# Optimization experiments

Hardware: AMD Instinct MI355X
Metric: run time of the kernel (lower is better)

## Reference

```python
import jax, jax.numpy as jnp
import numpy as np
import math


def setup_inputs() -> dict:
    key = jax.random.key(0)
    ks = jax.random.split(key, 8)
    B, C, H, W = 8, 512, 48, 48
    Cq = C // 8
    s = 0.05
    return {
        "x": jax.random.normal(ks[0], (B, C, H, W), jnp.float32),
        "Wq": jax.random.normal(ks[1], (Cq, C), jnp.float32) * s,
        "bq": jax.random.normal(ks[2], (Cq,), jnp.float32) * s,
        "Wk": jax.random.normal(ks[3], (Cq, C), jnp.float32) * s,
        "bk": jax.random.normal(ks[4], (Cq,), jnp.float32) * s,
        "Wv": jax.random.normal(ks[5], (C, C), jnp.float32) * s,
        "bv": jax.random.normal(ks[6], (C,), jnp.float32) * s,
        "gamma": jax.random.normal(ks[7], (1,), jnp.float32),
    }


def reference(x, Wq, bq, Wk, bk, Wv, bv, gamma):
    B, C, H, W = x.shape
    Cq = Wq.shape[0]
    N = H * W
    xf = x.reshape(B, C, N)  # 1x1 conv == channel matmul
    q = jnp.einsum('oc,bcn->bno', Wq, xf) + bq  # [B, N, Cq] (proj_query, permuted)
    k = jnp.einsum('oc,bcn->bon', Wk, xf) + bk[None, :, None]  # [B, Cq, N]
    v = jnp.einsum('oc,bcn->bon', Wv, xf) + bv[None, :, None]  # [B, C, N]
    # ave_I = (1/Cq)*(I - (1/Cq)*J); Q @ ave_I = (Q - rowmean(Q)) / Cq
    qc = (q - jnp.mean(q, axis=-1, keepdims=True)) / Cq
    sigma = jnp.einsum('bnc,bcm->bnm', qc, k) / math.sqrt(Cq)  # [B, N, N]
    attention = jax.nn.softmax(sigma, axis=-1)
    # out = V @ attention^T : out[b,c,n] = sum_m v[b,c,m] * attention[b,n,m]
    am = jnp.einsum('bcm,bnm->bcn', v, attention).reshape(B, C, H, W)
    out = gamma[0] * am + x
    return out
```

## Files before the change

kernel.cpp:

```cpp
#include <hip/hip_runtime.h>

#define B_ 8
#define C_ 512
#define N_ 2304
#define CQ 64

typedef float f32x4 __attribute__((ext_vector_type(4)));
typedef float f32x16 __attribute__((ext_vector_type(16)));
typedef short bf16x8 __attribute__((ext_vector_type(8)));
typedef unsigned short u16x4 __attribute__((ext_vector_type(4)));
typedef unsigned short u16x8 __attribute__((ext_vector_type(8)));
typedef int i32x4 __attribute__((ext_vector_type(4)));

__device__ __forceinline__ unsigned short f2bf(float f){
  union { float f; unsigned int u; } v; v.f = f;
  unsigned int r = (v.u + 0x7fffu + ((v.u >> 16) & 1u)) >> 16;
  return (unsigned short)r;
}

__device__ __forceinline__ void gload_lds16(const void* g, void* l){
  __builtin_amdgcn_global_load_lds(
      (const __attribute__((address_space(1))) unsigned int*)g,
      (__attribute__((address_space(3))) unsigned int*)l, 16, 0, 0);
}

__global__ __launch_bounds__(256) void k_wcvt(const float* __restrict__ Wq,
                                              const float* __restrict__ Wk,
                                              const float* __restrict__ Wv,
                                              unsigned short* __restrict__ Wb){
  int idx = blockIdx.x*256 + threadIdx.x;
  int h = idx & 1, ln = (idx >> 1) & 31, cs = (idx >> 6) & 31, ob = idx >> 11;
  int row = ob*32 + ln, col = cs*16 + h*8;
  const float* src;
  if (row < 64)       src = Wq + (size_t)row*512 + col;
  else if (row < 128) src = Wk + (size_t)(row-64)*512 + col;
  else                src = Wv + (size_t)(row-128)*512 + col;
  f32x4 v0 = *(const f32x4*)src;
  f32x4 v1 = *(const f32x4*)(src + 4);
  u16x8 o;
  #pragma unroll
  for (int j = 0; j < 4; j++){ o[j] = f2bf(v0[j]); o[4+j] = f2bf(v1[j]); }
  *(u16x8*)(Wb + (size_t)idx*8) = o;
}

__global__ __launch_bounds__(512) void k_prep(const float* __restrict__ x,
                                              const float* __restrict__ bq,
                                              const float* __restrict__ bk,
                                              const float* __restrict__ bv,
                                              const unsigned short* __restrict__ Wb,
                                              unsigned short* __restrict__ qw,
                                              unsigned short* __restrict__ kw,
                                              unsigned short* __restrict__ vw){
  __shared__ short xt_l[32*520];
  __shared__ float scr[2*32*68];

  int i = blockIdx.x; int b = i & 7; int nt = i >> 3;
  int n0 = nt*32;
  int t = threadIdx.x; int w = t >> 6; int l = t & 63;
  int h = l >> 5, ln = l & 31;
  const size_t bN = (size_t)b*N_;

  #pragma unroll
  for (int it = 0; it < 8; it++){
    int c = it*64 + (t >> 3);
    int n4 = (t & 7)*4;
    f32x4 v = *(const f32x4*)(x + ((size_t)b*C_ + c)*N_ + n0 + n4);
    #pragma unroll
    for (int j = 0; j < 4; j++) xt_l[(n4+j)*520 + c] = (short)f2bf(v[j]);
  }
  __syncthreads();

  const unsigned short* wlane = Wb + (size_t)(ln*2 + h)*8;
  const unsigned short* wv0 = wlane + (size_t)(4 + 2*w)*16384;
  const unsigned short* wv1 = wlane + (size_t)(5 + 2*w)*16384;
  const unsigned short* wqk = wlane + (size_t)w*16384;

  f32x16 vacc[2]; f32x16 qkacc;
  #pragma unroll
  for (int rr = 0; rr < 16; rr++){ vacc[0][rr]=0.f; vacc[1][rr]=0.f; qkacc[rr]=0.f; }

  #pragma unroll 8
  for (int cs = 0; cs < 32; cs++){
    bf16x8 bx = *(const bf16x8*)&xt_l[ln*520 + cs*16 + h*8];
    bf16x8 a0 = *(const bf16x8*)(wv0 + (size_t)cs*512);
    bf16x8 a1 = *(const bf16x8*)(wv1 + (size_t)cs*512);
    vacc[0] = __builtin_amdgcn_mfma_f32_32x32x16_bf16(a0, bx, vacc[0], 0, 0, 0);
    vacc[1] = __builtin_amdgcn_mfma_f32_32x32x16_bf16(a1, bx, vacc[1], 0, 0, 0);
    if (w < 4){
      bf16x8 aq = *(const bf16x8*)(wqk + (size_t)cs*512);
      qkacc = __builtin_amdgcn_mfma_f32_32x32x16_bf16(aq, bx, qkacc, 0, 0, 0);
    }
  }

  if (w < 4){
    float* s = scr + ((w >> 1) ? 2176 : 0);
    int obase = (w & 1)*32;
    #pragma unroll
    for (int rr = 0; rr < 16; rr++){
      int o = obase + (rr & 3) + 8*(rr >> 2) + 4*h;
      s[ln*68 + o] = qkacc[rr];
    }
  }
  __syncthreads();

  if (t < 256){
    int isK = t >> 7;
    int tt = t & 127;
    int n = tt >> 2, j = tt & 3;
    const float* s = scr + (isK ? 2176 : 0);
    const float* bias = isK ? bk : bq;
    float vals[16]; float sm = 0.f;
    #pragma unroll
    for (int ii = 0; ii < 16; ii++){
      vals[ii] = s[n*68 + j*16 + ii] + bias[j*16 + ii];
      sm += vals[ii];
    }
    sm += __shfl_xor(sm, 1); sm += __shfl_xor(sm, 2);
    float mean = isK ? 0.f : sm * (1.f/64.f);
    float scl  = isK ? 1.f : (1.44269504089f/512.f);
    u16x8 h0, h1;
    #pragma unroll
    for (int ii = 0; ii < 8; ii++) h0[ii] = f2bf((vals[ii]   - mean)*scl);
    #pragma unroll
    for (int ii = 0; ii < 8; ii++) h1[ii] = f2bf((vals[8+ii] - mean)*scl);
    unsigned short* d = (isK ? kw : qw) + (bN + n0 + n)*CQ + j*16;
    *(u16x8*)d = h0;
    *(u16x8*)(d + 8) = h1;
  }
  __syncthreads();

  #pragma unroll
  for (int r = 0; r < 4; r++){
    if ((w >> 1) == r){
      float* s = scr + (w & 1)*2176;
      #pragma unroll
      for (int of = 0; of < 2; of++)
        #pragma unroll
        for (int rr = 0; rr < 16; rr++){
          int o = of*32 + (rr & 3) + 8*(rr >> 2) + 4*h;
          s[ln*68 + o] = vacc[of][rr];
        }
    }
    __syncthreads();
    {
      int ch = t >> 8;
      int tt = t & 255;
      int o = tt >> 2, jj = (tt >> 1) & 1, half = tt & 1;
      int og = (2*r + ch)*64 + o;
      const float* s = scr + ch*2176;
      float bvv = bv[og];
      u16x8 hv;
      #pragma unroll
      for (int ii = 0; ii < 8; ii++){
        int q2 = ((ii & 3) | ((ii & 4) << 1)) + half*4;
        hv[ii] = f2bf(s[(jj*16 + q2)*68 + o] + bvv);
      }
      *(u16x8*)(vw + ((size_t)b*C_ + og)*N_ + n0 + jj*16 + half*8) = hv;
    }
    __syncthreads();
  }
}

__global__ __launch_bounds__(256) void k_sexp(const unsigned short* __restrict__ qw,
                                              const unsigned short* __restrict__ kw,
                                              unsigned short* __restrict__ Pl,
                                              float* __restrict__ lsum_part,
                                              int b0, int bsh){
  int bid = blockIdx.x;
  int bl = bid & ((1 << bsh) - 1);
  int b = b0 + bl;
  int r = bid >> bsh;
  int ms = r & 3; int nt = r >> 2;
  int t = threadIdx.x; int w = t >> 6; int l = t & 63;
  int h = l >> 5, ln = l & 31;
  int nf = w & 1, mh = w >> 1;
  int n = nt*64 + nf*32 + ln;

  const unsigned short* qb = qw + ((size_t)b*N_ + n)*CQ + h*8;
  bf16x8 qf[4];
  #pragma unroll
  for (int kq = 0; kq < 4; kq++) qf[kq] = *(const bf16x8*)(qb + kq*16);

  int mb32base = ms*18 + mh*9;
  const unsigned short* ks0 = kw + ((size_t)b*N_ + ln)*CQ + h*8 + (size_t)mb32base*32*CQ;
  unsigned short* pb = Pl + ((size_t)bl*144*N_ + n)*16 + h*8;

  float lsum = 0.f;
  bf16x8 ka[4], kc[4];
  #pragma unroll
  for (int kq = 0; kq < 4; kq++) ka[kq] = *(const bf16x8*)(ks0 + kq*16);

  #define SEXP_BODY(MF, KF, KN, PFOFF)                                          \
  {                                                                             \
    _Pragma("unroll")                                                           \
    for (int kq = 0; kq < 4; kq++)                                              \
      KN[kq] = *(const bf16x8*)(ks0 + (size_t)(PFOFF)*32*CQ + kq*16);           \
    f32x16 sv;                                                                  \
    _Pragma("unroll")                                                           \
    for (int rr = 0; rr < 16; rr++) sv[rr] = 0.f;                               \
    _Pragma("unroll")                                                           \
    for (int kq = 0; kq < 4; kq++)                                              \
      sv = __builtin_amdgcn_mfma_f32_32x32x16_bf16(KF[kq], qf[kq], sv, 0, 0, 0);\
    float e[16];                                                                \
    _Pragma("unroll")                                                           \
    for (int rr = 0; rr < 16; rr++) e[rr] = exp2f(sv[rr]);                      \
    _Pragma("unroll")                                                           \
    for (int rr = 0; rr < 16; rr++) lsum += e[rr];                              \
    unsigned int pd[8];                                                         \
    _Pragma("unroll")                                                           \
    for (int j = 0; j < 8; j++)                                                 \
      asm("v_cvt_pk_bf16_f32 %0, %1, %2" : "=v"(pd[j]) : "v"(e[2*j]), "v"(e[2*j+1])); \
    i32x4 lo = (i32x4){(int)pd[0],(int)pd[1],(int)pd[2],(int)pd[3]};            \
    i32x4 hi = (i32x4){(int)pd[4],(int)pd[5],(int)pd[6],(int)pd[7]};            \
    unsigned short* d = pb + (size_t)((mb32base + (MF))*2)*N_*16;               \
    *(i32x4*)d = lo;                                                            \
    *(i32x4*)(d + (size_t)N_*16) = hi;                                          \
  }

  #pragma unroll
  for (int it = 0; it < 4; it++){
    SEXP_BODY(2*it,     ka, kc, 2*it + 1)
    SEXP_BODY(2*it + 1, kc, ka, 2*it + 2)
  }
  SEXP_BODY(8, ka, kc, 8)
  #undef SEXP_BODY

  lsum += __shfl_xor(lsum, 32);
  if (l < 32)
    lsum_part[((size_t)bl*8 + ms*2 + mh)*N_ + n] = lsum;
}

__global__ __launch_bounds__(256, 1) void k_pv(const unsigned short* __restrict__ vw,
                                               const unsigned short* __restrict__ Pl,
                                               const float* __restrict__ lsum_part,
                                               const float* __restrict__ x,
                                               const float* __restrict__ gamma_p,
                                               float* __restrict__ out,
                                               int b0, int bsh){
  __shared__ __attribute__((aligned(16))) short At[3][128*64];

  int bid = blockIdx.x;
  int bl = bid & ((1 << bsh) - 1);
  int b = b0 + bl;
  int r = bid >> bsh;
  int cb = r & 3; int nb = r >> 2;
  int c0 = cb*128, n0g = nb*128;
  int t = threadIdx.x; int w = t >> 6; int l = t & 63;
  int h = l >> 5, ln = l & 31;
  int wc = w & 1, wn = w >> 1;

  int gc = ((l & 7) - (l >> 3)) & 7;
  const unsigned short* asrc0 = vw + ((size_t)b*C_ + c0 + w*32 + (l >> 3))*N_ + gc*8;
  int aro[2][4];
  #pragma unroll
  for (int cf = 0; cf < 2; cf++)
    #pragma unroll
    for (int mb = 0; mb < 4; mb++){
      int row = wc*64 + cf*32 + ln;
      aro[cf][mb] = (row*8 + ((mb*2 + h + row) & 7)) * 16;
    }
  const unsigned short* Pb = Pl + (size_t)bl*144*N_*16;
  size_t bstep = (size_t)N_*16;
  int boff[2];
  #pragma unroll
  for (int nf = 0; nf < 2; nf++)
    boff[nf] = (n0g + wn*64 + nf*32 + ln)*16 + h*8;

  f32x16 acc[2][2];
  #pragma unroll
  for (int cf = 0; cf < 2; cf++)
    #pragma unroll
    for (int nf = 0; nf < 2; nf++)
      #pragma unroll
      for (int rr = 0; rr < 16; rr++) acc[cf][nf][rr] = 0.f;

  bf16x8 B0[2][4], B1[2][4], B2[2][4];

  #pragma unroll
  for (int j = 0; j < 4; j++)
    gload_lds16(asrc0 + (size_t)j*8*N_, &At[0][w*2048 + j*512]);
  #pragma unroll
  for (int j = 0; j < 4; j++)
    gload_lds16(asrc0 + (size_t)j*8*N_ + 64, &At[1][w*2048 + j*512]);
  #pragma unroll
  for (int nf = 0; nf < 2; nf++)
    #pragma unroll
    for (int mb = 0; mb < 4; mb++)
      B0[nf][mb] = *(const bf16x8*)(Pb + (size_t)mb*bstep + boff[nf]);
  #pragma unroll
  for (int nf = 0; nf < 2; nf++)
    #pragma unroll
    for (int mb = 0; mb < 4; mb++)
      B1[nf][mb] = *(const bf16x8*)(Pb + (size_t)(4 + mb)*bstep + boff[nf]);
  asm volatile("s_waitcnt vmcnt(20)" ::: "memory");
  __builtin_amdgcn_s_barrier();
  __builtin_amdgcn_sched_barrier(0);

  #define PV_STEP(KT, RD, WR, BC, BN)                                           \
  {                                                                             \
    const char* Ab = (const char*)At[RD];                                       \
    bf16x8 a_[2][4];                                                            \
    _Pragma("unroll")                                                           \
    for (int cf = 0; cf < 2; cf++)                                              \
      _Pragma("unroll")                                                         \
      for (int mb = 0; mb < 4; mb++)                                            \
        a_[cf][mb] = *(const bf16x8*)(Ab + aro[cf][mb]);                        \
    int m2 = ((KT) + 2 < 36) ? ((KT) + 2)*64 : 0;                               \
    _Pragma("unroll")                                                           \
    for (int j = 0; j < 4; j++)                                                 \
      gload_lds16(asrc0 + (size_t)j*8*N_ + m2, &At[WR][w*2048 + j*512]);        \
    {                                                                           \
      size_t mb2 = (size_t)((((KT) + 2 < 36) ? ((KT) + 2)*4 : 0));              \
      _Pragma("unroll")                                                         \
      for (int nf = 0; nf < 2; nf++)                                            \
        _Pragma("unroll")                                                       \
        for (int mb = 0; mb < 4; mb++)                                          \
          BN[nf][mb] = *(const bf16x8*)(Pb + (mb2 + mb)*bstep + boff[nf]);      \
    }                                                                           \
    _Pragma("unroll")                                                           \
    for (int cf = 0; cf < 2; cf++)                                              \
      _Pragma("unroll")                                                         \
      for (int nf = 0; nf < 2; nf++)                                            \
        _Pragma("unroll")                                                       \
        for (int mb = 0; mb < 4; mb++)                                          \
          acc[cf][nf] = __builtin_amdgcn_mfma_f32_32x32x16_bf16(                \
              a_[cf][mb], BC[nf][mb], acc[cf][nf], 0, 0, 0);                    \
    asm volatile("s_waitcnt vmcnt(20) lgkmcnt(0)" ::: "memory");                \
    __builtin_amdgcn_s_barrier();                                               \
    __builtin_amdgcn_sched_barrier(0);                                          \
  }

  for (int it = 0; it < 6; it++){
    int kt = it*6;
    PV_STEP(kt+0, 0, 2, B0, B2)
    PV_STEP(kt+1, 1, 0, B1, B0)
    PV_STEP(kt+2, 2, 1, B2, B1)
    PV_STEP(kt+3, 0, 2, B0, B2)
    PV_STEP(kt+4, 1, 0, B1, B0)
    PV_STEP(kt+5, 2, 1, B2, B1)
  }
  #undef PV_STEP

  float gmv = gamma_p[0];
  #pragma unroll
  for (int nf = 0; nf < 2; nf++){
    int n = n0g + wn*64 + nf*32 + ln;
    float s = 0.f;
    #pragma unroll
    for (int j = 0; j < 8; j++) s += lsum_part[((size_t)bl*8 + j)*N_ + n];
    float f = gmv / s;
    #pragma unroll
    for (int cf = 0; cf < 2; cf++){
      #pragma unroll
      for (int rr = 0; rr < 16; rr++){
        int c = c0 + wc*64 + cf*32 + (rr & 3) + 8*(rr >> 2) + 4*h;
        size_t idx = ((size_t)b*C_ + c)*N_ + n;
        out[idx] = acc[cf][nf][rr]*f + x[idx];
      }
    }
  }
}

extern "C" void kernel_launch(void* const* d_in, const int* in_sizes, int n_in,
                              void* d_out, int out_size, void* d_ws, size_t ws_size,
                              hipStream_t stream) {
  (void)in_sizes; (void)n_in; (void)out_size;
  const float* x  = (const float*)d_in[0];
  const float* Wq = (const float*)d_in[1];
  const float* bq = (const float*)d_in[2];
  const float* Wk = (const float*)d_in[3];
  const float* bk = (const float*)d_in[4];
  const float* Wv = (const float*)d_in[5];
  const float* bv = (const float*)d_in[6];
  const float* gm = (const float*)d_in[7];
  float* out = (float*)d_out;

  const size_t qw_b = (size_t)B_*N_*CQ*2;
  const size_t vw_b = (size_t)B_*C_*N_*2;
  const size_t wb_b = (size_t)640*512*2;

  int nbg = 8, bsh = 3;
  for (;;){
    size_t pl_b   = (size_t)nbg*144*N_*16*2;
    size_t lsum_b = (size_t)nbg*8*N_*4;
    size_t need   = pl_b + 2*qw_b + vw_b + lsum_b + wb_b;
    if (need <= ws_size || nbg == 1) break;
    nbg >>= 1; bsh--;
  }
  size_t pl_b   = (size_t)nbg*144*N_*16*2;
  size_t lsum_b = (size_t)nbg*8*N_*4;

  char* wsc = (char*)d_ws;
  unsigned short* Pl = (unsigned short*)wsc;
  unsigned short* qw = (unsigned short*)(wsc + pl_b);
  unsigned short* kw = (unsigned short*)(wsc + pl_b + qw_b);
  unsigned short* vw = (unsigned short*)(wsc + pl_b + 2*qw_b);
  float* lsum_part   = (float*)(wsc + pl_b + 2*qw_b + vw_b);
  unsigned short* Wb = (unsigned short*)(wsc + pl_b + 2*qw_b + vw_b + lsum_b);

  k_wcvt<<<160, 256, 0, stream>>>(Wq, Wk, Wv, Wb);
  k_prep<<<576, 512, 0, stream>>>(x, bq, bk, bv, Wb, qw, kw, vw);

  for (int b0 = 0; b0 < B_; b0 += nbg){
    k_sexp<<<144*nbg, 256, 0, stream>>>(qw, kw, Pl, lsum_part, b0, bsh);
    k_pv<<<72*nbg, 256, 0, stream>>>(vw, Pl, lsum_part, x, gm, out, b0, bsh);
  }
}
```

Baseline: 130.1 us.

## Make PV A-tiles wave-private to drop block barriers and reuse double buffer

Each wave in the PV kernel now loads its own 64-row slice of V into a private LDS region, so no cross-wave sharing is needed and the per-step s_barrier is removed. The ring shrinks from three shared buffers to two per-wave buffers, with waits on vmcnt and lgkmcnt instead of a block barrier. MFMA sections are wrapped in s_setprio, and the launch bound no longer forces one block per CU. The cost is that waves sharing a channel half now load the same V rows twice, doubling global-to-LDS traffic for A, and a buffer is overwritten right after it is read, which relies on lgkmcnt(0) ordering.

```diff
diff --git a/kernel.cpp b/kernel.cpp
--- a/kernel.cpp
+++ b/kernel.cpp
@@ -230,14 +230,14 @@
     lsum_part[((size_t)bl*8 + ms*2 + mh)*N_ + n] = lsum;
 }
 
-__global__ __launch_bounds__(256, 1) void k_pv(const unsigned short* __restrict__ vw,
-                                               const unsigned short* __restrict__ Pl,
-                                               const float* __restrict__ lsum_part,
-                                               const float* __restrict__ x,
-                                               const float* __restrict__ gamma_p,
-                                               float* __restrict__ out,
-                                               int b0, int bsh){
-  __shared__ __attribute__((aligned(16))) short At[3][128*64];
+__global__ __launch_bounds__(256) void k_pv(const unsigned short* __restrict__ vw,
+                                            const unsigned short* __restrict__ Pl,
+                                            const float* __restrict__ lsum_part,
+                                            const float* __restrict__ x,
+                                            const float* __restrict__ gamma_p,
+                                            float* __restrict__ out,
+                                            int b0, int bsh){
+  __shared__ __attribute__((aligned(16))) short At[2][4][4096];
 
   int bid = blockIdx.x;
   int bl = bid & ((1 << bsh) - 1);
@@ -250,14 +250,15 @@
   int wc = w & 1, wn = w >> 1;
 
   int gc = ((l & 7) - (l >> 3)) & 7;
-  const unsigned short* asrc0 = vw + ((size_t)b*C_ + c0 + w*32 + (l >> 3))*N_ + gc*8;
+  const unsigned short* asrc0 = vw + ((size_t)b*C_ + c0 + wc*64 + (l >> 3))*N_ + gc*8;
+  short* aw[2] = { At[0][w], At[1][w] };
   int aro[2][4];
   #pragma unroll
   for (int cf = 0; cf < 2; cf++)
     #pragma unroll
     for (int mb = 0; mb < 4; mb++){
-      int row = wc*64 + cf*32 + ln;
-      aro[cf][mb] = (row*8 + ((mb*2 + h + row) & 7)) * 16;
+      int rr_ = cf*32 + ln;
+      aro[cf][mb] = (rr_*8 + ((mb*2 + h + rr_) & 7)) * 16;
     }
   const unsigned short* Pb = Pl + (size_t)bl*144*N_*16;
   size_t bstep = (size_t)N_*16;
@@ -277,38 +278,39 @@
   bf16x8 B0[2][4], B1[2][4], B2[2][4];
 
   #pragma unroll
-  for (int j = 0; j < 4; j++)
-    gload_lds16(asrc0 + (size_t)j*8*N_, &At[0][w*2048 + j*512]);
-  #pragma unroll
-  for (int j = 0; j < 4; j++)
-    gload_lds16(asrc0 + (size_t)j*8*N_ + 64, &At[1][w*2048 + j*512]);
+  for (int j = 0; j < 8; j++)
+    gload_lds16(asrc0 + (size_t)j*8*N_, aw[0] + j*512);
   #pragma unroll
   for (int nf = 0; nf < 2; nf++)
     #pragma unroll
     for (int mb = 0; mb < 4; mb++)
       B0[nf][mb] = *(const bf16x8*)(Pb + (size_t)mb*bstep + boff[nf]);
   #pragma unroll
+  for (int j = 0; j < 8; j++)
+    gload_lds16(asrc0 + (size_t)j*8*N_ + 64, aw[1] + j*512);
+  #pragma unroll
   for (int nf = 0; nf < 2; nf++)
     #pragma unroll
     for (int mb = 0; mb < 4; mb++)
       B1[nf][mb] = *(const bf16x8*)(Pb + (size_t)(4 + mb)*bstep + boff[nf]);
-  asm volatile("s_waitcnt vmcnt(20)" ::: "memory");
-  __builtin_amdgcn_s_barrier();
-  __builtin_amdgcn_sched_barrier(0);
-
-  #define PV_STEP(KT, RD, WR, BC, BN)                                           \
+
+  #define PV_STEP(KT, P, BC, BN)                                                \
   {                                                                             \
-    const char* Ab = (const char*)At[RD];                                       \
+    asm volatile("s_waitcnt vmcnt(16)" ::: "memory");                           \
+    __builtin_amdgcn_sched_barrier(0);                                          \
+    const char* Ab = (const char*)aw[P];                                        \
     bf16x8 a_[2][4];                                                            \
     _Pragma("unroll")                                                           \
     for (int cf = 0; cf < 2; cf++)                                              \
       _Pragma("unroll")                                                         \
       for (int mb = 0; mb < 4; mb++)                                            \
         a_[cf][mb] = *(const bf16x8*)(Ab + aro[cf][mb]);                        \
+    asm volatile("s_waitcnt lgkmcnt(0)" ::: "memory");                          \
+    __builtin_amdgcn_sched_barrier(0);                                          \
     int m2 = ((KT) + 2 < 36) ? ((KT) + 2)*64 : 0;                               \
     _Pragma("unroll")                                                           \
-    for (int j = 0; j < 4; j++)                                                 \
-      gload_lds16(asrc0 + (size_t)j*8*N_ + m2, &At[WR][w*2048 + j*512]);        \
+    for (int j = 0; j < 8; j++)                                                 \
+      gload_lds16(asrc0 + (size_t)j*8*N_ + m2, aw[P] + j*512);                  \
     {                                                                           \
       size_t mb2 = (size_t)((((KT) + 2 < 36) ? ((KT) + 2)*4 : 0));              \
       _Pragma("unroll")                                                         \
@@ -317,6 +319,7 @@
         for (int mb = 0; mb < 4; mb++)                                          \
           BN[nf][mb] = *(const bf16x8*)(Pb + (mb2 + mb)*bstep + boff[nf]);      \
     }                                                                           \
+    __builtin_amdgcn_s_setprio(1);                                              \
     _Pragma("unroll")                                                           \
     for (int cf = 0; cf < 2; cf++)                                              \
       _Pragma("unroll")                                                         \
@@ -325,19 +328,17 @@
         for (int mb = 0; mb < 4; mb++)                                          \
           acc[cf][nf] = __builtin_amdgcn_mfma_f32_32x32x16_bf16(                \
               a_[cf][mb], BC[nf][mb], acc[cf][nf], 0, 0, 0);                    \
-    asm volatile("s_waitcnt vmcnt(20) lgkmcnt(0)" ::: "memory");                \
-    __builtin_amdgcn_s_barrier();                                               \
-    __builtin_amdgcn_sched_barrier(0);                                          \
+    __builtin_amdgcn_s_setprio(0);                                              \
   }
 
   for (int it = 0; it < 6; it++){
     int kt = it*6;
-    PV_STEP(kt+0, 0, 2, B0, B2)
-    PV_STEP(kt+1, 1, 0, B1, B0)
-    PV_STEP(kt+2, 2, 1, B2, B1)
-    PV_STEP(kt+3, 0, 2, B0, B2)
-    PV_STEP(kt+4, 1, 0, B1, B0)
-    PV_STEP(kt+5, 2, 1, B2, B1)
+    PV_STEP(kt+0, 0, B0, B2)
+    PV_STEP(kt+1, 1, B1, B0)
+    PV_STEP(kt+2, 0, B2, B1)
+    PV_STEP(kt+3, 1, B0, B2)
+    PV_STEP(kt+4, 0, B1, B0)
+    PV_STEP(kt+5, 1, B2, B1)
   }
   #undef PV_STEP
 
```

Result: slower. 149.4 us (+14.8%).
